# Optimization experiments

Measured on AMD Instinct MI355X. Metric: run time of the kernel, lower is better.

## Reference

```python
import jax, jax.numpy as jnp
import numpy as np

B, L, D = 2, 4096, 1024      # batch, seq_len, d_model (expand_ratio=1 -> d_inner == D)
DS, RK, K = 16, 64, 3        # d_state, dt_rank, conv kernel size
EPS = 1e-5


def setup_inputs() -> dict:
    key = jax.random.key(0)
    ks = jax.random.split(key, 16)
    s = 0.02
    inp = {
        "x":      jax.random.normal(ks[0], (B, L, D), jnp.float32),
        "gamma":  jnp.ones((D,), jnp.float32),
        "beta":   jnp.zeros((D,), jnp.float32),
        "W_in":   jax.random.normal(ks[1], (D, 2 * D), jnp.float32) * s,
        "conv_w": jax.random.normal(ks[2], (K, 1, D), jnp.float32) * s,   # depthwise (k, 1, d)
        "conv_b": jnp.zeros((D,), jnp.float32),
        "W_xp":   jax.random.normal(ks[3], (D, RK), jnp.float32) * s,
        "W_Bg":   jax.random.normal(ks[4], (D, DS), jnp.float32) * s,
        "W_Cg":   jax.random.normal(ks[5], (D, DS), jnp.float32) * s,
        "W_dt":   jax.random.normal(ks[6], (RK, D), jnp.float32) * s,
        "b_dt":   jnp.zeros((D,), jnp.float32),
        "W_Bp":   jax.random.normal(ks[7], (DS, D), jnp.float32) * s,
        "W_Cp":   jax.random.normal(ks[8], (DS, D), jnp.float32) * s,
        "A":      -jnp.exp(jax.random.normal(ks[9], (D,), jnp.float32) * 0.5),  # negative for stability
        "D_skip": jnp.ones((D,), jnp.float32),
        "W_out":  jax.random.normal(ks[10], (D, D), jnp.float32) * s,
    }
    return inp


def reference(x, gamma, beta, W_in, conv_w, conv_b, W_xp, W_Bg, W_Cg,
              W_dt, b_dt, W_Bp, W_Cp, A, D_skip, W_out):
    d = x.shape[-1]
    # 1. LayerNorm
    mu = jnp.mean(x, -1, keepdims=True)
    var = jnp.mean(jnp.square(x - mu), -1, keepdims=True)
    xn = (x - mu) * jax.lax.rsqrt(var + EPS) * gamma + beta
    # 2. in_proj + split into main/gate branch
    xz = xn @ W_in                                 # (b, l, 2d)
    xb, z = jnp.split(xz, 2, axis=-1)
    # 3. depthwise Conv1D (same padding) + SiLU
    xc = jax.lax.conv_general_dilated(
        xb, conv_w, window_strides=(1,), padding='SAME',
        dimension_numbers=('NWC', 'WIO', 'NWC'), feature_group_count=d) + conv_b
    x_act = jax.nn.silu(xc)                        # (b, l, d)
    # SSM parameter generation
    delta = jax.nn.softplus((x_act @ W_xp) @ W_dt + b_dt)   # (b, l, d)
    Bm = (x_act @ W_Bg) @ W_Bp                     # (b, l, d)
    Cm = (x_act @ W_Cg) @ W_Cp                     # (b, l, d)
    # 4. diagonal selective scan: h_t = exp(delta*A)*h_{t-1} + delta*B*x ; y = C*h
    dA = jnp.exp(delta * A)
    dBx = delta * Bm * x_act
    def step(h, ab):
        a, bx = ab
        h = a * h + bx
        return h, h
    h0 = jnp.zeros_like(dA[:, 0])
    _, hs = jax.lax.scan(step, h0, (dA.transpose(1, 0, 2), dBx.transpose(1, 0, 2)))
    y = Cm * hs.transpose(1, 0, 2)
    # 5. skip-D, gating, out_proj + residual
    out_ssm = y + x_act * D_skip
    gated = out_ssm * jax.nn.silu(z)
    return gated @ W_out + x
```

## Files before the change

kernel.cpp:

```cpp
#include <hip/hip_runtime.h>
#include <math.h>

#define BB 2
#define LL 4096
#define DD 1024
#define DS 16
#define RK 64
#define MM (BB*LL)
#define NC 128
#define LC (LL/NC)

typedef __attribute__((ext_vector_type(8))) short short8;
typedef __attribute__((ext_vector_type(4))) float f32x4;

__device__ __forceinline__ unsigned short f2bf(float f) {
    union { float f; unsigned u; } v; v.f = f;
    unsigned r = v.u + 0x7fff + ((v.u >> 16) & 1);
    return (unsigned short)(r >> 16);
}
__device__ __forceinline__ float bf2f(unsigned short u) {
    union { unsigned u; float f; } v; v.u = ((unsigned)u) << 16;
    return v.f;
}
__device__ __forceinline__ float2 bf2x2(unsigned u) {
    return make_float2(bf2f((unsigned short)u), bf2f((unsigned short)(u >> 16)));
}
__device__ __forceinline__ unsigned f2bfx2(float lo, float hi) {
    return (unsigned)f2bf(lo) | ((unsigned)f2bf(hi) << 16);
}
__device__ __forceinline__ float fast_rcp(float x) {
    return __builtin_amdgcn_rcpf(x);
}
__device__ __forceinline__ float silu_f(float v) {
    return v * fast_rcp(1.0f + __expf(-v));
}
__device__ __forceinline__ void gload16(const void* g, void* l) {
    __builtin_amdgcn_global_load_lds(
        (const __attribute__((address_space(1))) unsigned int*)g,
        (__attribute__((address_space(3))) unsigned int*)l, 16, 0, 0);
}

__global__ __launch_bounds__(256)
void ln_kernel(const float* __restrict__ x, const float* __restrict__ gamma,
               const float* __restrict__ beta, unsigned short* __restrict__ xn_bf) {
    int row = blockIdx.x;
    int tid = threadIdx.x;
    const float4* xr = (const float4*)(x + (size_t)row * DD);
    float4 v = xr[tid];
    float s = v.x + v.y + v.z + v.w;
    float q = v.x*v.x + v.y*v.y + v.z*v.z + v.w*v.w;
    #pragma unroll
    for (int off = 32; off > 0; off >>= 1) {
        s += __shfl_down(s, off);
        q += __shfl_down(q, off);
    }
    __shared__ float ss[4], qq[4];
    int wv = tid >> 6;
    if ((tid & 63) == 0) { ss[wv] = s; qq[wv] = q; }
    __syncthreads();
    float S = ss[0] + ss[1] + ss[2] + ss[3];
    float Q = qq[0] + qq[1] + qq[2] + qq[3];
    float mu  = S * (1.0f / DD);
    float var = Q * (1.0f / DD) - mu * mu;
    float r = rsqrtf(var + 1e-5f);
    int d0 = tid * 4;
    float4 gv = *(const float4*)(gamma + d0);
    float4 bv = *(const float4*)(beta + d0);
    ushort4 o;
    o.x = f2bf((v.x - mu) * r * gv.x + bv.x);
    o.y = f2bf((v.y - mu) * r * gv.y + bv.y);
    o.z = f2bf((v.z - mu) * r * gv.z + bv.z);
    o.w = f2bf((v.w - mu) * r * gv.w + bv.w);
    *(ushort4*)&xn_bf[(size_t)row * DD + d0] = o;
}

__global__ __launch_bounds__(256)
void prep_weights(const float* __restrict__ W_in, const float* __restrict__ W_out,
                  const float* __restrict__ W_xp, const float* __restrict__ W_Bg,
                  const float* __restrict__ W_Cg, const float* __restrict__ W_dt,
                  const float* __restrict__ W_Bp, const float* __restrict__ W_Cp,
                  unsigned short* __restrict__ WinT, unsigned short* __restrict__ WoutT,
                  unsigned short* __restrict__ WgT, unsigned short* __restrict__ WdtT,
                  float* __restrict__ WBpT, float* __restrict__ WCpT) {
    __shared__ float t[32][33];
    int b = blockIdx.x;
    if (b < 3072) {
        const float* W; unsigned short* WT; int K, N, n0, k0;
        if (b < 2048) { W = W_in;  WT = WinT;  K = DD; N = 2 * DD;
                        n0 = (b & 63) * 32; k0 = (b >> 6) * 32; }
        else { int bb = b - 2048; W = W_out; WT = WoutT; K = DD; N = DD;
               n0 = (bb & 31) * 32; k0 = (bb >> 5) * 32; }
        int tx = threadIdx.x & 31, ty = threadIdx.x >> 5;
        #pragma unroll
        for (int r = 0; r < 32; r += 8)
            t[ty + r][tx] = W[(size_t)(k0 + ty + r) * N + n0 + tx];
        __syncthreads();
        #pragma unroll
        for (int r = 0; r < 32; r += 8) {
            int nl = ty + r;
            WT[(size_t)(n0 + nl) * K + k0 + tx] = f2bf(t[tx][nl]);
        }
    } else if (b < 3584) {
        int idx = (b - 3072) * 256 + threadIdx.x;
        int k = idx & 1023, n = idx >> 10;
        float v = 0.0f;
        if (n < 64)       v = W_xp[k * RK + n];
        else if (n < 80)  v = W_Bg[k * DS + (n - 64)];
        else if (n < 96)  v = W_Cg[k * DS + (n - 80)];
        WgT[idx] = f2bf(v);
    } else if (b < 4096) {
        int idx = (b - 3584) * 256 + threadIdx.x;
        int k = idx & 127, n = idx >> 7;
        float v = (k < 64) ? W_dt[k * 1024 + n] : 0.0f;
        WdtT[idx] = f2bf(v);
    } else if (b < 4160) {
        int idx = (b - 4096) * 256 + threadIdx.x;
        WBpT[idx] = W_Bp[(idx & 15) * 1024 + (idx >> 4)];
    } else {
        int idx = (b - 4160) * 256 + threadIdx.x;
        WCpT[idx] = W_Cp[(idx & 15) * 1024 + (idx >> 4)];
    }
}

#define MF(a, b, c) __builtin_amdgcn_mfma_f32_16x16x32_bf16(a, b, c, 0, 0, 0)
template<int EPI>
__global__ __launch_bounds__(512, 1)
void gemm256(const unsigned short* __restrict__ A, const unsigned short* __restrict__ BT,
             void* __restrict__ C0v, void* __restrict__ C1v,
             const float* __restrict__ res, int M, int N, int K) {
    extern __shared__ unsigned short sm[];
    unsigned short* As = sm;
    unsigned short* Bs = sm + 32768;
    const int tid = threadIdx.x;
    const int wave = tid >> 6, lane = tid & 63;
    const int wr = wave >> 2, wc = wave & 3;
    const int fr = lane & 15, fs = lane >> 4;

    int nbx = gridDim.x;
    int nwg = nbx * gridDim.y;
    int bid = blockIdx.y * nbx + blockIdx.x;
    int cpx = nwg >> 3;
    int swz = (bid & 7) * cpx + (bid >> 3);
    int by = swz / nbx, bx = swz - by * nbx;
    size_t rb = (size_t)by * 256, cb = (size_t)bx * 256;

    const int srow = tid >> 3;
    const int ssw  = (tid & 7) ^ (srow & 7);
    const unsigned short* gA = A + (rb + srow) * K + ssw * 8;
    const unsigned short* gB = BT + (cb + srow) * K + ssw * 8;
    const size_t rstep = (size_t)64 * K;
    unsigned short* dA = As + tid * 8;
    unsigned short* dB = Bs + tid * 8;
    const int T = K >> 6;

#define STG(rnd, buf, kt) do { \
    gload16(gA + (size_t)(rnd) * rstep + (size_t)(kt) * 64, dA + (buf) * 16384 + (rnd) * 4096); \
    gload16(gB + (size_t)(rnd) * rstep + (size_t)(kt) * 64, dB + (buf) * 16384 + (rnd) * 4096); } while (0)
#define FOFF(r, S) (((r) << 6) + ((((S) ^ ((r) & 7))) << 3))
#define LDA(i, kk) (*(const short8*)&Ab[FOFF(arow0 + ((i) << 4), fs + ((kk) << 2))])
#define LDB(j, kk) (*(const short8*)&Bb[FOFF(brow0 + ((j) << 4), fs + ((kk) << 2))])

    const int arow0 = wr * 128 + fr;
    const int brow0 = wc * 64 + fr;

    f32x4 acc[8][4] = {};

    STG(0, 0, 0); STG(1, 0, 0); STG(2, 0, 0); STG(3, 0, 0);

    #pragma unroll 1
    for (int t = 0; t < T; ++t) {
        const int cur = t & 1, nx = cur ^ 1;
        const bool pf = (t + 1) < T;
        const unsigned short* Ab = As + cur * 16384;
        const unsigned short* Bb = Bs + cur * 16384;

        if (pf) { STG(0, nx, t + 1); }
        if (pf) { asm volatile("s_waitcnt vmcnt(2)" ::: "memory"); }
        else    { asm volatile("s_waitcnt vmcnt(0)" ::: "memory"); }
        __builtin_amdgcn_s_barrier();
        __builtin_amdgcn_sched_barrier(0);

        short8 bfr[4][2];
        #pragma unroll
        for (int j = 0; j < 4; ++j) {
            bfr[j][0] = LDB(j, 0);
            bfr[j][1] = LDB(j, 1);
        }
        __builtin_amdgcn_s_setprio(1);
        #pragma unroll
        for (int ii = 0; ii < 2; ++ii) {
            short8 a0 = LDA(ii, 0), a1 = LDA(ii, 1);
            #pragma unroll
            for (int j = 0; j < 4; ++j) {
                acc[ii][j] = MF(a0, bfr[j][0], acc[ii][j]);
                acc[ii][j] = MF(a1, bfr[j][1], acc[ii][j]);
            }
        }
        __builtin_amdgcn_s_setprio(0);
        __builtin_amdgcn_sched_barrier(0);

        #pragma unroll
        for (int p = 1; p < 4; ++p) {
            if (pf) { STG(p, nx, t + 1); }
            __builtin_amdgcn_s_setprio(1);
            #pragma unroll
            for (int ii = 0; ii < 2; ++ii) {
                const int i = 2 * p + ii;
                short8 a0 = LDA(i, 0), a1 = LDA(i, 1);
                #pragma unroll
                for (int j = 0; j < 4; ++j) {
                    acc[i][j] = MF(a0, bfr[j][0], acc[i][j]);
                    acc[i][j] = MF(a1, bfr[j][1], acc[i][j]);
                }
            }
            __builtin_amdgcn_s_setprio(0);
            __builtin_amdgcn_sched_barrier(0);
        }
        __builtin_amdgcn_s_barrier();
    }

    const int row0 = (int)rb + wr * 128 + fs * 4;
    const int col0 = (int)cb + wc * 64 + fr;
    if (EPI == 1) {
        unsigned short* Cd = (cb < DD) ? (unsigned short*)C0v : (unsigned short*)C1v;
        const int cadj = (cb < DD) ? 0 : -DD;
        #pragma unroll
        for (int i = 0; i < 8; ++i)
            #pragma unroll
            for (int j = 0; j < 4; ++j) {
                int col = col0 + cadj + (j << 4);
                #pragma unroll
                for (int q = 0; q < 4; ++q)
                    Cd[(size_t)(row0 + (i << 4) + q) * DD + col] = f2bf(acc[i][j][q]);
            }
    } else {
        float* C0 = (float*)C0v;
        #pragma unroll
        for (int i = 0; i < 8; ++i)
            #pragma unroll
            for (int j = 0; j < 4; ++j) {
                int col = col0 + (j << 4);
                #pragma unroll
                for (int q = 0; q < 4; ++q) {
                    size_t off = (size_t)(row0 + (i << 4) + q) * N + col;
                    C0[off] = acc[i][j][q] + res[off];
                }
            }
    }
#undef STG
#undef FOFF
#undef LDA
#undef LDB
}

__global__ __launch_bounds__(256)
void gemm_up(const unsigned short* __restrict__ A, const unsigned short* __restrict__ BT,
             unsigned short* __restrict__ C, const float* __restrict__ bias, int N) {
    __shared__ unsigned short As[128 * 128];
    __shared__ unsigned short Bs[128 * 128];
    int tid = threadIdx.x;
    int rb = blockIdx.y * 128, cb = blockIdx.x * 128;
    int wave = tid >> 6, lane = tid & 63;
    int wr = wave >> 1, wc = wave & 1;
    int fr = lane & 15, fs = lane >> 4;

    int srow16 = tid >> 4, sseg = tid & 15;
    #pragma unroll
    for (int r = 0; r < 8; ++r) {
        int row = r * 16 + srow16;
        int ss = sseg ^ (row & 15);
        gload16(A + (size_t)(rb + row) * 128 + ss * 8, (char*)As + r * 4096 + tid * 16);
        gload16(BT + (size_t)(cb + row) * 128 + ss * 8, (char*)Bs + r * 4096 + tid * 16);
    }
    asm volatile("s_waitcnt vmcnt(0)" ::: "memory");
    __syncthreads();

    f32x4 acc[4][4] = {};
    #pragma unroll
    for (int kk = 0; kk < 4; ++kk) {
        short8 af[4], bfr[4];
        #pragma unroll
        for (int i = 0; i < 4; ++i) {
            int row = (wr << 6) + (i << 4) + fr;
            int s = (fs + (kk << 2)) ^ (row & 15);
            af[i] = *(const short8*)&As[row * 128 + s * 8];
        }
        #pragma unroll
        for (int j = 0; j < 4; ++j) {
            int row = (wc << 6) + (j << 4) + fr;
            int s = (fs + (kk << 2)) ^ (row & 15);
            bfr[j] = *(const short8*)&Bs[row * 128 + s * 8];
        }
        #pragma unroll
        for (int i = 0; i < 4; ++i)
            #pragma unroll
            for (int j = 0; j < 4; ++j)
                acc[i][j] = MF(af[i], bfr[j], acc[i][j]);
    }

    int row0 = rb + (wr << 6) + (fs << 2);
    int col0 = (wc << 6) + fr;
    #pragma unroll
    for (int i = 0; i < 4; ++i)
        #pragma unroll
        for (int j = 0; j < 4; ++j) {
            int col = cb + col0 + (j << 4);
            float bv = bias[col];
            #pragma unroll
            for (int q = 0; q < 4; ++q) {
                float v = acc[i][j][q] + bv;
                v = fmaxf(v, 0.0f) + __logf(1.0f + __expf(-fabsf(v)));
                C[(size_t)(row0 + (i << 4) + q) * N + col] = f2bf(v);
            }
        }
}

__global__ __launch_bounds__(256)
void gemm_down(const unsigned short* __restrict__ A, const unsigned short* __restrict__ BT,
               unsigned short* __restrict__ C0, int M, int N, int K) {
    __shared__ unsigned short As[128 * 32];
    __shared__ unsigned short Bs[128 * 32];
    int tid = threadIdx.x;
    int rb = blockIdx.y * 128, cb = blockIdx.x * 128;
    int wave = tid >> 6, lane = tid & 63;
    int wr = wave >> 1, wc = wave & 1;
    int fr = lane & 15, fs = lane >> 4;

    int r0 = tid >> 2, s0 = tid & 3;
    int sw0 = s0 ^ ((r0 >> 1) & 3);
    const unsigned short* gA = A + (size_t)(rb + r0) * K + sw0 * 8;
    const unsigned short* gB = BT + (size_t)(cb + r0) * K + sw0 * 8;
    size_t half = (size_t)64 * K;
    char* lA0 = (char*)As + tid * 16;
    char* lA1 = (char*)As + (tid + 256) * 16;
    char* lB0 = (char*)Bs + tid * 16;
    char* lB1 = (char*)Bs + (tid + 256) * 16;

    int kb = blockIdx.z * (K >> 2), ke = kb + (K >> 2);

    f32x4 acc[4][4] = {};

    #pragma unroll 1
    for (int k0 = kb; k0 < ke; k0 += 32) {
        __syncthreads();
        gload16(gA + k0, lA0);
        gload16(gA + half + k0, lA1);
        gload16(gB + k0, lB0);
        gload16(gB + half + k0, lB1);
        __syncthreads();

        short8 af[4], bfr[4];
        #pragma unroll
        for (int i = 0; i < 4; i++) {
            int row = (wr << 6) + (i << 4) + fr;
            int off = (row << 5) + ((fs ^ ((row >> 1) & 3)) << 3);
            af[i] = *(const short8*)&As[off];
        }
        #pragma unroll
        for (int j = 0; j < 4; j++) {
            int row = (wc << 6) + (j << 4) + fr;
            int off = (row << 5) + ((fs ^ ((row >> 1) & 3)) << 3);
            bfr[j] = *(const short8*)&Bs[off];
        }
        #pragma unroll
        for (int i = 0; i < 4; i++)
            #pragma unroll
            for (int j = 0; j < 4; j++)
                acc[i][j] = MF(af[i], bfr[j], acc[i][j]);
    }

    int row0 = rb + (wr << 6) + (fs << 2);
    int col0 = (wc << 6) + fr;
    unsigned short* Cp = C0 + (size_t)blockIdx.z * M * N;
    #pragma unroll
    for (int i = 0; i < 4; i++)
        #pragma unroll
        for (int j = 0; j < 4; j++) {
            int col = cb + col0 + (j << 4);
            #pragma unroll
            for (int q = 0; q < 4; q++)
                Cp[(size_t)(row0 + (i << 4) + q) * N + col] = f2bf(acc[i][j][q]);
        }
}

__global__ __launch_bounds__(256)
void reduce_t(const unsigned short* __restrict__ tp, unsigned short* __restrict__ t_bf) {
    int idx = blockIdx.x * 256 + threadIdx.x;
    const size_t Q = (size_t)MM * 128;
    ushort4 a = ((const ushort4*)tp)[idx];
    ushort4 b = ((const ushort4*)(tp + Q))[idx];
    ushort4 c = ((const ushort4*)(tp + 2 * Q))[idx];
    ushort4 d = ((const ushort4*)(tp + 3 * Q))[idx];
    ushort4 o;
    o.x = f2bf(bf2f(a.x) + bf2f(b.x) + bf2f(c.x) + bf2f(d.x));
    o.y = f2bf(bf2f(a.y) + bf2f(b.y) + bf2f(c.y) + bf2f(d.y));
    o.z = f2bf(bf2f(a.z) + bf2f(b.z) + bf2f(c.z) + bf2f(d.z));
    o.w = f2bf(bf2f(a.w) + bf2f(b.w) + bf2f(c.w) + bf2f(d.w));
    ((ushort4*)t_bf)[idx] = o;
}

__global__ __launch_bounds__(256)
void conv_silu(const unsigned short* __restrict__ xb, const float* __restrict__ cw,
               const float* __restrict__ cb, unsigned short* __restrict__ xact) {
    int idx8 = blockIdx.x * 256 + threadIdx.x;
    size_t e = (size_t)idx8 * 8;
    int d0 = (int)(e & (DD - 1));
    int bl = (int)(e >> 10);
    int l = bl & (LL - 1);
    short8 cur = *(const short8*)&xb[e];
    short8 prv = {}, nxt = {};
    if (l > 0)      prv = *(const short8*)&xb[e - DD];
    if (l < LL - 1) nxt = *(const short8*)&xb[e + DD];
    short8 o;
    #pragma unroll
    for (int j = 0; j < 8; j++) {
        int d = d0 + j;
        float acc = cb[d];
        acc = fmaf(bf2f((unsigned short)prv[j]), cw[0 * DD + d], acc);
        acc = fmaf(bf2f((unsigned short)cur[j]), cw[1 * DD + d], acc);
        acc = fmaf(bf2f((unsigned short)nxt[j]), cw[2 * DD + d], acc);
        o[j] = (short)f2bf(silu_f(acc));
    }
    *(short8*)&xact[e] = o;
}

__global__ __launch_bounds__(256)
void scan_p1(const unsigned short* __restrict__ delta, const unsigned short* __restrict__ xact,
             const unsigned short* __restrict__ t_bf, const float* __restrict__ WBpT,
             const float* __restrict__ A, float* __restrict__ P, float* __restrict__ Hc) {
    __shared__ float tbs[LC][16];
    int tid = threadIdx.x;
    int d = (blockIdx.x * 256 + tid) * 2;
    int c = blockIdx.y, b = blockIdx.z;
    int row0 = b * LL + c * LC;
    {
        int rr = tid >> 3, kp = (tid & 7) * 2;
        float2 f = bf2x2(*(const unsigned*)&t_bf[(size_t)(row0 + rr) * 128 + 64 + kp]);
        tbs[rr][kp] = f.x; tbs[rr][kp + 1] = f.y;
    }
    __syncthreads();
    float wB0[16], wB1[16];
    #pragma unroll
    for (int j = 0; j < 4; ++j) {
        *(float4*)&wB0[j * 4] = *(const float4*)&WBpT[(size_t)d * 16 + j * 4];
        *(float4*)&wB1[j * 4] = *(const float4*)&WBpT[(size_t)(d + 1) * 16 + j * 4];
    }
    float2 a_d = *(const float2*)&A[d];
    float h0 = 0.0f, h1 = 0.0f, sd0 = 0.0f, sd1 = 0.0f;
    #pragma unroll 2
    for (int i = 0; i < LC; i++) {
        size_t o = (size_t)(row0 + i) * DD + d;
        float2 dl = bf2x2(*(const unsigned*)&delta[o]);
        float2 xa = bf2x2(*(const unsigned*)&xact[o]);
        float bm0 = 0.0f, bm1 = 0.0f;
        #pragma unroll
        for (int j = 0; j < 4; ++j) {
            float4 t4 = *(const float4*)&tbs[i][j * 4];
            bm0 = fmaf(t4.x, wB0[j*4+0], bm0); bm1 = fmaf(t4.x, wB1[j*4+0], bm1);
            bm0 = fmaf(t4.y, wB0[j*4+1], bm0); bm1 = fmaf(t4.y, wB1[j*4+1], bm1);
            bm0 = fmaf(t4.z, wB0[j*4+2], bm0); bm1 = fmaf(t4.z, wB1[j*4+2], bm1);
            bm0 = fmaf(t4.w, wB0[j*4+3], bm0); bm1 = fmaf(t4.w, wB1[j*4+3], bm1);
        }
        float a0 = __expf(dl.x * a_d.x);
        float a1 = __expf(dl.y * a_d.y);
        h0 = fmaf(a0, h0, dl.x * bm0 * xa.x);
        h1 = fmaf(a1, h1, dl.y * bm1 * xa.y);
        sd0 += dl.x; sd1 += dl.y;
    }
    int pc = (b * NC + c) * DD + d;
    *(float2*)&P[pc]  = make_float2(__expf(a_d.x * sd0), __expf(a_d.y * sd1));
    *(float2*)&Hc[pc] = make_float2(h0, h1);
}

__global__ __launch_bounds__(256)
void scan_p2(const float* __restrict__ P, const float* __restrict__ Hc,
             float* __restrict__ hin) {
    int d = blockIdx.x * 256 + threadIdx.x;
    int b = blockIdx.y;
    float carry = 0.0f;
    #pragma unroll 4
    for (int c = 0; c < NC; c++) {
        int o = (b * NC + c) * DD + d;
        hin[o] = carry;
        carry = fmaf(P[o], carry, Hc[o]);
    }
}

__global__ __launch_bounds__(256)
void scan_p3(const unsigned short* __restrict__ delta, const unsigned short* __restrict__ xact,
             const unsigned short* __restrict__ zb, const unsigned short* __restrict__ t_bf,
             const float* __restrict__ WBpT, const float* __restrict__ WCpT,
             const float* __restrict__ hin, const float* __restrict__ A,
             const float* __restrict__ Dsk, unsigned short* __restrict__ g) {
    __shared__ float tbs[LC][16];
    __shared__ float tcs[LC][16];
    int tid = threadIdx.x;
    int d = (blockIdx.x * 256 + tid) * 2;
    int c = blockIdx.y, b = blockIdx.z;
    int row0 = b * LL + c * LC;
    {
        int rr = tid >> 3, kp = (tid & 7) * 2;
        const unsigned short* tr = &t_bf[(size_t)(row0 + rr) * 128];
        float2 fb = bf2x2(*(const unsigned*)&tr[64 + kp]);
        float2 fc = bf2x2(*(const unsigned*)&tr[80 + kp]);
        tbs[rr][kp] = fb.x; tbs[rr][kp + 1] = fb.y;
        tcs[rr][kp] = fc.x; tcs[rr][kp + 1] = fc.y;
    }
    __syncthreads();
    float wB0[16], wB1[16], wC0[16], wC1[16];
    #pragma unroll
    for (int j = 0; j < 4; ++j) {
        *(float4*)&wB0[j * 4] = *(const float4*)&WBpT[(size_t)d * 16 + j * 4];
        *(float4*)&wB1[j * 4] = *(const float4*)&WBpT[(size_t)(d + 1) * 16 + j * 4];
        *(float4*)&wC0[j * 4] = *(const float4*)&WCpT[(size_t)d * 16 + j * 4];
        *(float4*)&wC1[j * 4] = *(const float4*)&WCpT[(size_t)(d + 1) * 16 + j * 4];
    }
    float2 a_d = *(const float2*)&A[d];
    float2 dsk = *(const float2*)&Dsk[d];
    float2 hv = *(const float2*)&hin[(b * NC + c) * DD + d];
    float h0 = hv.x, h1 = hv.y;
    #pragma unroll 2
    for (int i = 0; i < LC; i++) {
        size_t o = (size_t)(row0 + i) * DD + d;
        float2 dl = bf2x2(*(const unsigned*)&delta[o]);
        float2 xa = bf2x2(*(const unsigned*)&xact[o]);
        float2 zv = bf2x2(*(const unsigned*)&zb[o]);
        float bm0 = 0.0f, bm1 = 0.0f, cm0 = 0.0f, cm1 = 0.0f;
        #pragma unroll
        for (int j = 0; j < 4; ++j) {
            float4 t4 = *(const float4*)&tbs[i][j * 4];
            float4 c4 = *(const float4*)&tcs[i][j * 4];
            bm0 = fmaf(t4.x, wB0[j*4+0], bm0); bm1 = fmaf(t4.x, wB1[j*4+0], bm1);
            bm0 = fmaf(t4.y, wB0[j*4+1], bm0); bm1 = fmaf(t4.y, wB1[j*4+1], bm1);
            bm0 = fmaf(t4.z, wB0[j*4+2], bm0); bm1 = fmaf(t4.z, wB1[j*4+2], bm1);
            bm0 = fmaf(t4.w, wB0[j*4+3], bm0); bm1 = fmaf(t4.w, wB1[j*4+3], bm1);
            cm0 = fmaf(c4.x, wC0[j*4+0], cm0); cm1 = fmaf(c4.x, wC1[j*4+0], cm1);
            cm0 = fmaf(c4.y, wC0[j*4+1], cm0); cm1 = fmaf(c4.y, wC1[j*4+1], cm1);
            cm0 = fmaf(c4.z, wC0[j*4+2], cm0); cm1 = fmaf(c4.z, wC1[j*4+2], cm1);
            cm0 = fmaf(c4.w, wC0[j*4+3], cm0); cm1 = fmaf(c4.w, wC1[j*4+3], cm1);
        }
        float a0 = __expf(dl.x * a_d.x);
        float a1 = __expf(dl.y * a_d.y);
        h0 = fmaf(a0, h0, dl.x * bm0 * xa.x);
        h1 = fmaf(a1, h1, dl.y * bm1 * xa.y);
        float os0 = fmaf(xa.x, dsk.x, cm0 * h0);
        float os1 = fmaf(xa.y, dsk.y, cm1 * h1);
        float g0 = os0 * silu_f(zv.x);
        float g1 = os1 * silu_f(zv.y);
        *(unsigned*)&g[o] = f2bfx2(g0, g1);
    }
}

extern "C" void kernel_launch(void* const* d_in, const int* in_sizes, int n_in,
                              void* d_out, int out_size, void* d_ws, size_t ws_size,
                              hipStream_t stream) {
    const float* x      = (const float*)d_in[0];
    const float* gamma  = (const float*)d_in[1];
    const float* beta   = (const float*)d_in[2];
    const float* W_in   = (const float*)d_in[3];
    const float* conv_w = (const float*)d_in[4];
    const float* conv_b = (const float*)d_in[5];
    const float* W_xp   = (const float*)d_in[6];
    const float* W_Bg   = (const float*)d_in[7];
    const float* W_Cg   = (const float*)d_in[8];
    const float* W_dt   = (const float*)d_in[9];
    const float* b_dt   = (const float*)d_in[10];
    const float* W_Bp   = (const float*)d_in[11];
    const float* W_Cp   = (const float*)d_in[12];
    const float* A      = (const float*)d_in[13];
    const float* Dsk    = (const float*)d_in[14];
    const float* W_out  = (const float*)d_in[15];
    float* out = (float*)d_out;

    const size_t BIG = (size_t)MM * DD;
    char* p = (char*)d_ws;
    unsigned short* xn_bf   = (unsigned short*)p;  p += BIG * 2;
    unsigned short* xb_bf   = (unsigned short*)p;  p += BIG * 2;
    unsigned short* z_bf    = (unsigned short*)p;  p += BIG * 2;
    unsigned short* xact_bf = (unsigned short*)p;  p += BIG * 2;
    unsigned short* delta_bf= (unsigned short*)p;  p += BIG * 2;
    unsigned short* t_bf    = (unsigned short*)p;  p += (size_t)MM * 128 * 2;
    unsigned short* tpart   = (unsigned short*)p;  p += (size_t)4 * MM * 128 * 2;
    float* P     = (float*)p;                      p += (size_t)BB * NC * DD * 4;
    float* Hc    = (float*)p;                      p += (size_t)BB * NC * DD * 4;
    float* hin   = (float*)p;                      p += (size_t)BB * NC * DD * 4;
    unsigned short* WinT  = (unsigned short*)p;    p += (size_t)2 * DD * DD * 2;
    unsigned short* WoutT = (unsigned short*)p;    p += (size_t)DD * DD * 2;
    unsigned short* WgT   = (unsigned short*)p;    p += (size_t)128 * DD * 2;
    unsigned short* WdtT  = (unsigned short*)p;    p += (size_t)DD * 128 * 2;
    float* WBpT = (float*)p;                       p += (size_t)DD * 16 * 4;
    float* WCpT = (float*)p;                       p += (size_t)DD * 16 * 4;
    unsigned short* g_bf  = xn_bf;

    {
        void (*k1)(const unsigned short*, const unsigned short*, void*, void*,
                   const float*, int, int, int) = gemm256<1>;
        void (*k2)(const unsigned short*, const unsigned short*, void*, void*,
                   const float*, int, int, int) = gemm256<2>;
        (void)hipFuncSetAttribute((const void*)k1,
            hipFuncAttributeMaxDynamicSharedMemorySize, 131072);
        (void)hipFuncSetAttribute((const void*)k2,
            hipFuncAttributeMaxDynamicSharedMemorySize, 131072);
    }

    prep_weights<<<4224, 256, 0, stream>>>(W_in, W_out, W_xp, W_Bg, W_Cg,
                                           W_dt, W_Bp, W_Cp,
                                           WinT, WoutT, WgT, WdtT, WBpT, WCpT);
    ln_kernel<<<MM, 256, 0, stream>>>(x, gamma, beta, xn_bf);
    gemm256<1><<<dim3(2 * DD / 256, MM / 256), 512, 131072, stream>>>(
        xn_bf, WinT, xb_bf, z_bf, nullptr, MM, 2 * DD, DD);
    conv_silu<<<(MM * DD / 8) / 256, 256, 0, stream>>>(xb_bf, conv_w, conv_b, xact_bf);
    gemm_down<<<dim3(1, MM / 128, 4), 256, 0, stream>>>(
        xact_bf, WgT, tpart, MM, 128, DD);
    reduce_t<<<(MM * 128 / 4) / 256, 256, 0, stream>>>(tpart, t_bf);
    gemm_up<<<dim3(DD / 128, MM / 128), 256, 0, stream>>>(
        t_bf, WdtT, delta_bf, b_dt, DD);
    scan_p1<<<dim3(DD / 512, NC, BB), 256, 0, stream>>>(delta_bf, xact_bf, t_bf,
                                                        WBpT, A, P, Hc);
    scan_p2<<<dim3(DD / 256, BB), 256, 0, stream>>>(P, Hc, hin);
    scan_p3<<<dim3(DD / 512, NC, BB), 256, 0, stream>>>(delta_bf, xact_bf, z_bf, t_bf,
                                                        WBpT, WCpT, hin, A, Dsk, g_bf);
    gemm256<2><<<dim3(DD / 256, MM / 256), 512, 131072, stream>>>(
        g_bf, WoutT, out, nullptr, x, MM, DD, DD);
}
```

Baseline: 177.5 us.

## Fuse weight prep with LayerNorm, use 128-row tiles for out_proj, stage scan carry in LDS

```diff
diff --git a/kernel.cpp b/kernel.cpp
--- a/kernel.cpp
+++ b/kernel.cpp
@@ -41,50 +41,48 @@
 }
 
 __global__ __launch_bounds__(256)
-void ln_kernel(const float* __restrict__ x, const float* __restrict__ gamma,
+void prep_misc(const float* __restrict__ W_in, const float* __restrict__ W_out,
+               const float* __restrict__ W_xp, const float* __restrict__ W_Bg,
+               const float* __restrict__ W_Cg, const float* __restrict__ W_dt,
+               const float* __restrict__ W_Bp, const float* __restrict__ W_Cp,
+               unsigned short* __restrict__ WinT, unsigned short* __restrict__ WoutT,
+               unsigned short* __restrict__ WgT, unsigned short* __restrict__ WdtT,
+               float* __restrict__ WBpT, float* __restrict__ WCpT,
+               const float* __restrict__ x, const float* __restrict__ gamma,
                const float* __restrict__ beta, unsigned short* __restrict__ xn_bf) {
-    int row = blockIdx.x;
-    int tid = threadIdx.x;
-    const float4* xr = (const float4*)(x + (size_t)row * DD);
-    float4 v = xr[tid];
-    float s = v.x + v.y + v.z + v.w;
-    float q = v.x*v.x + v.y*v.y + v.z*v.z + v.w*v.w;
-    #pragma unroll
-    for (int off = 32; off > 0; off >>= 1) {
-        s += __shfl_down(s, off);
-        q += __shfl_down(q, off);
-    }
+    __shared__ float t[32][33];
     __shared__ float ss[4], qq[4];
-    int wv = tid >> 6;
-    if ((tid & 63) == 0) { ss[wv] = s; qq[wv] = q; }
-    __syncthreads();
-    float S = ss[0] + ss[1] + ss[2] + ss[3];
-    float Q = qq[0] + qq[1] + qq[2] + qq[3];
-    float mu  = S * (1.0f / DD);
-    float var = Q * (1.0f / DD) - mu * mu;
-    float r = rsqrtf(var + 1e-5f);
-    int d0 = tid * 4;
-    float4 gv = *(const float4*)(gamma + d0);
-    float4 bv = *(const float4*)(beta + d0);
-    ushort4 o;
-    o.x = f2bf((v.x - mu) * r * gv.x + bv.x);
-    o.y = f2bf((v.y - mu) * r * gv.y + bv.y);
-    o.z = f2bf((v.z - mu) * r * gv.z + bv.z);
-    o.w = f2bf((v.w - mu) * r * gv.w + bv.w);
-    *(ushort4*)&xn_bf[(size_t)row * DD + d0] = o;
-}
-
-__global__ __launch_bounds__(256)
-void prep_weights(const float* __restrict__ W_in, const float* __restrict__ W_out,
-                  const float* __restrict__ W_xp, const float* __restrict__ W_Bg,
-                  const float* __restrict__ W_Cg, const float* __restrict__ W_dt,
-                  const float* __restrict__ W_Bp, const float* __restrict__ W_Cp,
-                  unsigned short* __restrict__ WinT, unsigned short* __restrict__ WoutT,
-                  unsigned short* __restrict__ WgT, unsigned short* __restrict__ WdtT,
-                  float* __restrict__ WBpT, float* __restrict__ WCpT) {
-    __shared__ float t[32][33];
     int b = blockIdx.x;
-    if (b < 3072) {
+    if (b >= 4224) {
+        int row = b - 4224;
+        int tid = threadIdx.x;
+        const float4* xr = (const float4*)(x + (size_t)row * DD);
+        float4 v = xr[tid];
+        float s = v.x + v.y + v.z + v.w;
+        float q = v.x*v.x + v.y*v.y + v.z*v.z + v.w*v.w;
+        #pragma unroll
+        for (int off = 32; off > 0; off >>= 1) {
+            s += __shfl_down(s, off);
+            q += __shfl_down(q, off);
+        }
+        int wv = tid >> 6;
+        if ((tid & 63) == 0) { ss[wv] = s; qq[wv] = q; }
+        __syncthreads();
+        float S = ss[0] + ss[1] + ss[2] + ss[3];
+        float Q = qq[0] + qq[1] + qq[2] + qq[3];
+        float mu  = S * (1.0f / DD);
+        float var = Q * (1.0f / DD) - mu * mu;
+        float r = rsqrtf(var + 1e-5f);
+        int d0 = tid * 4;
+        float4 gv = *(const float4*)(gamma + d0);
+        float4 bv = *(const float4*)(beta + d0);
+        ushort4 o;
+        o.x = f2bf((v.x - mu) * r * gv.x + bv.x);
+        o.y = f2bf((v.y - mu) * r * gv.y + bv.y);
+        o.z = f2bf((v.z - mu) * r * gv.z + bv.z);
+        o.w = f2bf((v.w - mu) * r * gv.w + bv.w);
+        *(ushort4*)&xn_bf[(size_t)row * DD + d0] = o;
+    } else if (b < 3072) {
         const float* W; unsigned short* WT; int K, N, n0, k0;
         if (b < 2048) { W = W_in;  WT = WinT;  K = DD; N = 2 * DD;
                         n0 = (b & 63) * 32; k0 = (b >> 6) * 32; }
@@ -123,14 +121,17 @@
 }
 
 #define MF(a, b, c) __builtin_amdgcn_mfma_f32_16x16x32_bf16(a, b, c, 0, 0, 0)
-template<int EPI>
+template<int EPI, int BM>
 __global__ __launch_bounds__(512, 1)
 void gemm256(const unsigned short* __restrict__ A, const unsigned short* __restrict__ BT,
              void* __restrict__ C0v, void* __restrict__ C1v,
              const float* __restrict__ res, int M, int N, int K) {
+    constexpr int MR = BM / 32;
+    constexpr int RA = BM / 64;
+    constexpr int ABUF = BM * 64;
     extern __shared__ unsigned short sm[];
     unsigned short* As = sm;
-    unsigned short* Bs = sm + 32768;
+    unsigned short* Bs = sm + 2 * ABUF;
     const int tid = threadIdx.x;
     const int wave = tid >> 6, lane = tid & 63;
     const int wr = wave >> 2, wc = wave & 3;
@@ -142,7 +143,7 @@
     int cpx = nwg >> 3;
     int swz = (bid & 7) * cpx + (bid >> 3);
     int by = swz / nbx, bx = swz - by * nbx;
-    size_t rb = (size_t)by * 256, cb = (size_t)bx * 256;
+    size_t rb = (size_t)by * BM, cb = (size_t)bx * 256;
 
     const int srow = tid >> 3;
     const int ssw  = (tid & 7) ^ (srow & 7);
@@ -153,28 +154,30 @@
     unsigned short* dB = Bs + tid * 8;
     const int T = K >> 6;
 
-#define STG(rnd, buf, kt) do { \
-    gload16(gA + (size_t)(rnd) * rstep + (size_t)(kt) * 64, dA + (buf) * 16384 + (rnd) * 4096); \
-    gload16(gB + (size_t)(rnd) * rstep + (size_t)(kt) * 64, dB + (buf) * 16384 + (rnd) * 4096); } while (0)
+#define STGA(rnd, buf, kt) gload16(gA + (size_t)(rnd) * rstep + (size_t)(kt) * 64, dA + (buf) * ABUF + (rnd) * 4096)
+#define STGB(rnd, buf, kt) gload16(gB + (size_t)(rnd) * rstep + (size_t)(kt) * 64, dB + (buf) * 16384 + (rnd) * 4096)
 #define FOFF(r, S) (((r) << 6) + ((((S) ^ ((r) & 7))) << 3))
 #define LDA(i, kk) (*(const short8*)&Ab[FOFF(arow0 + ((i) << 4), fs + ((kk) << 2))])
 #define LDB(j, kk) (*(const short8*)&Bb[FOFF(brow0 + ((j) << 4), fs + ((kk) << 2))])
 
-    const int arow0 = wr * 128 + fr;
+    const int arow0 = wr * (BM / 2) + fr;
     const int brow0 = wc * 64 + fr;
 
-    f32x4 acc[8][4] = {};
-
-    STG(0, 0, 0); STG(1, 0, 0); STG(2, 0, 0); STG(3, 0, 0);
+    f32x4 acc[MR][4] = {};
+
+    #pragma unroll
+    for (int r = 0; r < RA; ++r) STGA(r, 0, 0);
+    #pragma unroll
+    for (int r = 0; r < 4; ++r) STGB(r, 0, 0);
 
     #pragma unroll 1
     for (int t = 0; t < T; ++t) {
         const int cur = t & 1, nx = cur ^ 1;
         const bool pf = (t + 1) < T;
-        const unsigned short* Ab = As + cur * 16384;
+        const unsigned short* Ab = As + cur * ABUF;
         const unsigned short* Bb = Bs + cur * 16384;
 
-        if (pf) { STG(0, nx, t + 1); }
+        if (pf) { STGA(0, nx, t + 1); STGB(0, nx, t + 1); }
         if (pf) { asm volatile("s_waitcnt vmcnt(2)" ::: "memory"); }
         else    { asm volatile("s_waitcnt vmcnt(0)" ::: "memory"); }
         __builtin_amdgcn_s_barrier();
@@ -188,7 +191,7 @@
         }
         __builtin_amdgcn_s_setprio(1);
         #pragma unroll
-        for (int ii = 0; ii < 2; ++ii) {
+        for (int ii = 0; ii < MR / 4; ++ii) {
             short8 a0 = LDA(ii, 0), a1 = LDA(ii, 1);
             #pragma unroll
             for (int j = 0; j < 4; ++j) {
@@ -201,11 +204,14 @@
 
         #pragma unroll
         for (int p = 1; p < 4; ++p) {
-            if (pf) { STG(p, nx, t + 1); }
+            if (pf) {
+                if (p < RA) STGA(p, nx, t + 1);
+                STGB(p, nx, t + 1);
+            }
             __builtin_amdgcn_s_setprio(1);
             #pragma unroll
-            for (int ii = 0; ii < 2; ++ii) {
-                const int i = 2 * p + ii;
+            for (int ii = 0; ii < MR / 4; ++ii) {
+                const int i = p * (MR / 4) + ii;
                 short8 a0 = LDA(i, 0), a1 = LDA(i, 1);
                 #pragma unroll
                 for (int j = 0; j < 4; ++j) {
@@ -219,13 +225,13 @@
         __builtin_amdgcn_s_barrier();
     }
 
-    const int row0 = (int)rb + wr * 128 + fs * 4;
+    const int row0 = (int)rb + wr * (BM / 2) + fs * 4;
     const int col0 = (int)cb + wc * 64 + fr;
     if (EPI == 1) {
         unsigned short* Cd = (cb < DD) ? (unsigned short*)C0v : (unsigned short*)C1v;
         const int cadj = (cb < DD) ? 0 : -DD;
         #pragma unroll
-        for (int i = 0; i < 8; ++i)
+        for (int i = 0; i < MR; ++i)
             #pragma unroll
             for (int j = 0; j < 4; ++j) {
                 int col = col0 + cadj + (j << 4);
@@ -236,7 +242,7 @@
     } else {
         float* C0 = (float*)C0v;
         #pragma unroll
-        for (int i = 0; i < 8; ++i)
+        for (int i = 0; i < MR; ++i)
             #pragma unroll
             for (int j = 0; j < 4; ++j) {
                 int col = col0 + (j << 4);
@@ -247,7 +253,8 @@
                 }
             }
     }
-#undef STG
+#undef STGA
+#undef STGB
 #undef FOFF
 #undef LDA
 #undef LDB
@@ -475,14 +482,32 @@
 __global__ __launch_bounds__(256)
 void scan_p2(const float* __restrict__ P, const float* __restrict__ Hc,
              float* __restrict__ hin) {
-    int d = blockIdx.x * 256 + threadIdx.x;
+    extern __shared__ float sP[];
+    float* sH = sP + NC * 128;
     int b = blockIdx.y;
-    float carry = 0.0f;
-    #pragma unroll 4
-    for (int c = 0; c < NC; c++) {
-        int o = (b * NC + c) * DD + d;
-        hin[o] = carry;
-        carry = fmaf(P[o], carry, Hc[o]);
+    int d0 = blockIdx.x * 128;
+    for (int idx = threadIdx.x; idx < NC * 128; idx += 256) {
+        int c = idx >> 7, dd = idx & 127;
+        int o = (b * NC + c) * DD + d0 + dd;
+        sP[idx] = P[o];
+        sH[idx] = Hc[o];
+    }
+    __syncthreads();
+    if (threadIdx.x < 128) {
+        int dd = threadIdx.x;
+        float carry = 0.0f;
+        #pragma unroll 4
+        for (int c = 0; c < NC; ++c) {
+            float pv = sP[c * 128 + dd];
+            float hv = sH[c * 128 + dd];
+            sP[c * 128 + dd] = carry;
+            carry = fmaf(pv, carry, hv);
+        }
+    }
+    __syncthreads();
+    for (int idx = threadIdx.x; idx < NC * 128; idx += 256) {
+        int c = idx >> 7, dd = idx & 127;
+        hin[(b * NC + c) * DD + d0 + dd] = sP[idx];
     }
 }
 
@@ -594,20 +619,23 @@
 
     {
         void (*k1)(const unsigned short*, const unsigned short*, void*, void*,
-                   const float*, int, int, int) = gemm256<1>;
+                   const float*, int, int, int) = gemm256<1, 256>;
         void (*k2)(const unsigned short*, const unsigned short*, void*, void*,
-                   const float*, int, int, int) = gemm256<2>;
+                   const float*, int, int, int) = gemm256<2, 128>;
+        void (*k3)(const float*, const float*, float*) = scan_p2;
         (void)hipFuncSetAttribute((const void*)k1,
             hipFuncAttributeMaxDynamicSharedMemorySize, 131072);
         (void)hipFuncSetAttribute((const void*)k2,
+            hipFuncAttributeMaxDynamicSharedMemorySize, 98304);
+        (void)hipFuncSetAttribute((const void*)k3,
             hipFuncAttributeMaxDynamicSharedMemorySize, 131072);
     }
 
-    prep_weights<<<4224, 256, 0, stream>>>(W_in, W_out, W_xp, W_Bg, W_Cg,
-                                           W_dt, W_Bp, W_Cp,
-                                           WinT, WoutT, WgT, WdtT, WBpT, WCpT);
-    ln_kernel<<<MM, 256, 0, stream>>>(x, gamma, beta, xn_bf);
-    gemm256<1><<<dim3(2 * DD / 256, MM / 256), 512, 131072, stream>>>(
+    prep_misc<<<4224 + MM, 256, 0, stream>>>(W_in, W_out, W_xp, W_Bg, W_Cg,
+                                             W_dt, W_Bp, W_Cp,
+                                             WinT, WoutT, WgT, WdtT, WBpT, WCpT,
+                                             x, gamma, beta, xn_bf);
+    gemm256<1, 256><<<dim3(2 * DD / 256, MM / 256), 512, 131072, stream>>>(
         xn_bf, WinT, xb_bf, z_bf, nullptr, MM, 2 * DD, DD);
     conv_silu<<<(MM * DD / 8) / 256, 256, 0, stream>>>(xb_bf, conv_w, conv_b, xact_bf);
     gemm_down<<<dim3(1, MM / 128, 4), 256, 0, stream>>>(
@@ -617,9 +645,9 @@
         t_bf, WdtT, delta_bf, b_dt, DD);
     scan_p1<<<dim3(DD / 512, NC, BB), 256, 0, stream>>>(delta_bf, xact_bf, t_bf,
                                                         WBpT, A, P, Hc);
-    scan_p2<<<dim3(DD / 256, BB), 256, 0, stream>>>(P, Hc, hin);
+    scan_p2<<<dim3(DD / 128, BB), 256, 131072, stream>>>(P, Hc, hin);
     scan_p3<<<dim3(DD / 512, NC, BB), 256, 0, stream>>>(delta_bf, xact_bf, z_bf, t_bf,
                                                         WBpT, WCpT, hin, A, Dsk, g_bf);
-    gemm256<2><<<dim3(DD / 256, MM / 256), 512, 131072, stream>>>(
+    gemm256<2, 128><<<dim3(DD / 256, MM / 128), 512, 98304, stream>>>(
         g_bf, WoutT, out, nullptr, x, MM, DD, DD);
 }
```

After: 158.3 us. -10.8%, faster.
